# Kernel tuning notes

Hardware: AMD Instinct MI355X
Metric: run time of the kernel (lower is better)

Reference implementation:

```python
import jax, jax.numpy as jnp
import numpy as np

T_LATENCY = 2  # refractory latency (timesteps), from init_kwargs
FS_SCALE = 10.0  # FastSigmoid surrogate scale


@jax.custom_vjp
def fast_sigmoid_spike(u):
    return (u > 0).astype(u.dtype)

def _fs_fwd(u):
    return fast_sigmoid_spike(u), u

def _fs_bwd(u, g):
    return (g / (FS_SCALE * jnp.abs(u) + 1.0) ** 2,)

fast_sigmoid_spike.defvjp(_fs_fwd, _fs_bwd)


def setup_inputs() -> dict:
    key = jax.random.key(0)
    k1, k2, k3, k4 = jax.random.split(key, 4)
    B, N, T = 64, 1024, 512
    x = jax.random.normal(k1, (B, N, T), dtype=jnp.float32)
    beta = jax.random.uniform(k2, (N,), jnp.float32, 0.3, 0.95)   # leak
    p = jax.random.uniform(k3, (N,), jnp.float32, 0.5, 0.95)      # adaptation decay
    b = jax.random.uniform(k4, (N,), jnp.float32, 0.5, 1.5)       # adaptation strength
    return {"x": x, "beta": beta, "p": p, "b": b}


def reference(x, beta, p, b):
    # clamped effective params (matches torch @property accessors)
    beta_c = jnp.clip(beta, 0.001, 0.999)
    p_c = jnp.clip(jnp.abs(p), 0.0, 0.999)
    b_c = jnp.clip(jnp.abs(b), 0.001, 1.0)

    B, N, T = x.shape
    xt = jnp.moveaxis(x, 2, 0)  # [T, B, N]

    def step(carry, x_t):
        mem, spikes, refac, a, v_th = carry
        # spike-triggered refractory reset, then mask input during refractory window
        refac = jnp.where(spikes > 0, 0.0, refac)
        ic = jnp.where(refac < T_LATENCY, 0.0, x_t)
        refac = refac + 1.0
        # leaky integration
        new_mem = mem * beta_c + ic
        s = fast_sigmoid_spike(new_mem - v_th)
        # reset-by-subtraction-to-zero with detached spikes (detach_spike_grad=True)
        mem = new_mem * (1.0 - jax.lax.stop_gradient(s))
        # adaptive threshold
        a = p_c * a + s
        v_th = 1.0 + b_c * a
        return (mem, s, refac, a, v_th), s

    z = jnp.zeros((B, N), x.dtype)
    init = (z, z, jnp.full((B, N), float(T_LATENCY), x.dtype), z,
            jnp.ones((B, N), x.dtype))
    _, spikes_seq = jax.lax.scan(step, init, xt)  # [T, B, N]
    return jnp.moveaxis(spikes_seq, 0, 2)  # [B, N, T]
```

## Files before the change

kernel.cpp:

```cpp
#include <hip/hip_runtime.h>

#pragma clang fp contract(off)

#define ROWS    64
#define T_LEN   512
#define CHUNK   64
#define NCHUNK  (T_LEN / CHUNK)
#define STRIDE  (CHUNK + 4)
#define NVEC    (ROWS * CHUNK / 4 / ROWS)
#define NPARAM  1024

__global__ __launch_bounds__(ROWS) void snn_fwd(
    const float* __restrict__ x,
    const float* __restrict__ beta,
    const float* __restrict__ p,
    const float* __restrict__ bparam,
    float* __restrict__ out)
{
    __shared__ float inbuf[ROWS * STRIDE];
    __shared__ float outbuf[ROWS * STRIDE];

    const int tid     = threadIdx.x;
    const int rowBase = blockIdx.x * ROWS;
    const int n       = (rowBase + tid) & (NPARAM - 1);

    const float beta_c = fminf(fmaxf(beta[n], 0.001f), 0.999f);
    const float p_c    = fminf(fabsf(p[n]), 0.999f);
    const float b_c    = fminf(fmaxf(fabsf(bparam[n]), 0.001f), 1.0f);

    float mem = 0.0f, refac = 2.0f, a = 0.0f, vth = 1.0f, ps = 0.0f;

    const float4* __restrict__ xv = (const float4*)x;
    float4* __restrict__ ov       = (float4*)out;

    const int t4c   = tid & 15;
    const int rquad = tid >> 4;
    const int gq    = (rowBase + rquad) * (T_LEN / 4) + t4c;
    const int lq    = rquad * STRIDE + t4c * 4;

    float4 ld[NVEC];

    auto loadChunk = [&](int k) {
        const int base = gq + k * (CHUNK / 4);
        #pragma unroll
        for (int it = 0; it < NVEC; ++it)
            ld[it] = xv[base + it * 4 * (T_LEN / 4)];
    };

    auto stage = [&]() {
        #pragma unroll
        for (int it = 0; it < NVEC; ++it)
            *(float4*)&inbuf[lq + it * 4 * STRIDE] = ld[it];
    };

    auto readout = [&](int k) {
        const int base = gq + k * (CHUNK / 4);
        #pragma unroll
        for (int it = 0; it < NVEC; ++it) {
            float4 sv = *(const float4*)&outbuf[lq + it * 4 * STRIDE];
            ov[base + it * 4 * (T_LEN / 4)] = sv;
        }
    };

    auto step = [&](float xt) -> float {
        refac = (ps > 0.0f) ? 0.0f : refac;
        const float ic = (refac < 2.0f) ? 0.0f : xt;
        refac += 1.0f;
        const float nm   = __fadd_rn(__fmul_rn(mem, beta_c), ic);
        const float diff = __fsub_rn(nm, vth);
        const float s    = (diff > 0.0f) ? 1.0f : 0.0f;
        mem = (diff > 0.0f) ? 0.0f : nm;
        a   = __fadd_rn(__fmul_rn(p_c, a), s);
        vth = __fadd_rn(1.0f, __fmul_rn(b_c, a));
        ps  = s;
        return s;
    };

    loadChunk(0);
    const int cbase = tid * STRIDE;

    #pragma unroll 1
    for (int k = 0; k < NCHUNK; ++k) {
        stage();
        if (k > 0) readout(k - 1);
        __syncthreads();
        if (k + 1 < NCHUNK) loadChunk(k + 1);
        #pragma unroll
        for (int t4 = 0; t4 < CHUNK / 4; ++t4) {
            float4 xq = *(const float4*)&inbuf[cbase + t4 * 4];
            float4 sv;
            sv.x = step(xq.x);
            sv.y = step(xq.y);
            sv.z = step(xq.z);
            sv.w = step(xq.w);
            *(float4*)&outbuf[cbase + t4 * 4] = sv;
        }
        __syncthreads();
    }
    readout(NCHUNK - 1);
}

extern "C" void kernel_launch(void* const* d_in, const int* in_sizes, int n_in,
                              void* d_out, int out_size, void* d_ws, size_t ws_size,
                              hipStream_t stream) {
    const float* x    = (const float*)d_in[0];
    const float* beta = (const float*)d_in[1];
    const float* p    = (const float*)d_in[2];
    const float* b    = (const float*)d_in[3];
    float* out        = (float*)d_out;

    const int BN = 64 * 1024;
    snn_fwd<<<dim3(BN / ROWS), dim3(ROWS), 0, stream>>>(x, beta, p, b, out);
}
```

Baseline: 260.9 us.

## Warp-specialize block into compute, loader and store wavefronts with double buffering

The block grows from one to three wavefronts. Wave 0 runs the serial recurrence, wave 1 prefetches and stages the next input chunk into a double-buffered shared array, and wave 2 drains the previous output chunk to global memory. The chunk size is halved to 32 timesteps. The goal is to take global load and store latency off the compute wave's critical path, at the cost of extra threads, twice the shared memory and more block barriers per row group.

```diff
diff --git a/kernel.cpp b/kernel.cpp
--- a/kernel.cpp
+++ b/kernel.cpp
@@ -4,63 +4,45 @@
 
 #define ROWS    64
 #define T_LEN   512
-#define CHUNK   64
+#define CHUNK   32
 #define NCHUNK  (T_LEN / CHUNK)
 #define STRIDE  (CHUNK + 4)
-#define NVEC    (ROWS * CHUNK / 4 / ROWS)
+#define NV      8
 #define NPARAM  1024
 
-__global__ __launch_bounds__(ROWS) void snn_fwd(
+__global__ __launch_bounds__(192) void snn_fwd(
     const float* __restrict__ x,
     const float* __restrict__ beta,
     const float* __restrict__ p,
     const float* __restrict__ bparam,
     float* __restrict__ out)
 {
-    __shared__ float inbuf[ROWS * STRIDE];
-    __shared__ float outbuf[ROWS * STRIDE];
+    __shared__ __align__(16) float inbuf [2][ROWS * STRIDE];
+    __shared__ __align__(16) float outbuf[2][ROWS * STRIDE];
 
     const int tid     = threadIdx.x;
+    const int wid     = tid >> 6;
+    const int lane    = tid & 63;
     const int rowBase = blockIdx.x * ROWS;
-    const int n       = (rowBase + tid) & (NPARAM - 1);
-
-    const float beta_c = fminf(fmaxf(beta[n], 0.001f), 0.999f);
-    const float p_c    = fminf(fabsf(p[n]), 0.999f);
-    const float b_c    = fminf(fmaxf(fabsf(bparam[n]), 0.001f), 1.0f);
-
-    float mem = 0.0f, refac = 2.0f, a = 0.0f, vth = 1.0f, ps = 0.0f;
 
     const float4* __restrict__ xv = (const float4*)x;
     float4* __restrict__ ov       = (float4*)out;
 
-    const int t4c   = tid & 15;
-    const int rquad = tid >> 4;
-    const int gq    = (rowBase + rquad) * (T_LEN / 4) + t4c;
-    const int lq    = rquad * STRIDE + t4c * 4;
+    const int t8 = lane & 7;
+    const int r8 = lane >> 3;
+    const int gq = (rowBase + r8) * (T_LEN / 4) + t8;
+    const int lq = r8 * STRIDE + t8 * 4;
 
-    float4 ld[NVEC];
+    float mem = 0.0f, refac = 2.0f, a = 0.0f, vth = 1.0f, ps = 0.0f;
+    float beta_c = 0.f, p_c = 0.f, b_c = 0.f;
+    const int cbase = lane * STRIDE;
 
-    auto loadChunk = [&](int k) {
-        const int base = gq + k * (CHUNK / 4);
-        #pragma unroll
-        for (int it = 0; it < NVEC; ++it)
-            ld[it] = xv[base + it * 4 * (T_LEN / 4)];
-    };
-
-    auto stage = [&]() {
-        #pragma unroll
-        for (int it = 0; it < NVEC; ++it)
-            *(float4*)&inbuf[lq + it * 4 * STRIDE] = ld[it];
-    };
-
-    auto readout = [&](int k) {
-        const int base = gq + k * (CHUNK / 4);
-        #pragma unroll
-        for (int it = 0; it < NVEC; ++it) {
-            float4 sv = *(const float4*)&outbuf[lq + it * 4 * STRIDE];
-            ov[base + it * 4 * (T_LEN / 4)] = sv;
-        }
-    };
+    if (wid == 0) {
+        const int n = (rowBase + lane) & (NPARAM - 1);
+        beta_c = fminf(fmaxf(beta[n], 0.001f), 0.999f);
+        p_c    = fminf(fabsf(p[n]), 0.999f);
+        b_c    = fminf(fmaxf(fabsf(bparam[n]), 0.001f), 1.0f);
+    }
 
     auto step = [&](float xt) -> float {
         refac = (ps > 0.0f) ? 0.0f : refac;
@@ -76,28 +58,60 @@
         return s;
     };
 
-    loadChunk(0);
-    const int cbase = tid * STRIDE;
+    float4 ld[NV];
+
+    auto loadChunk = [&](int k) {
+        const int base = gq + k * (CHUNK / 4);
+        #pragma unroll
+        for (int it = 0; it < NV; ++it)
+            ld[it] = xv[base + it * 8 * (T_LEN / 4)];
+    };
+    auto stage = [&](int buf) {
+        #pragma unroll
+        for (int it = 0; it < NV; ++it)
+            *(float4*)&inbuf[buf][lq + it * 8 * STRIDE] = ld[it];
+    };
+    auto drain = [&](int buf, int k) {
+        float4 sv[NV];
+        #pragma unroll
+        for (int it = 0; it < NV; ++it)
+            sv[it] = *(const float4*)&outbuf[buf][lq + it * 8 * STRIDE];
+        const int base = gq + k * (CHUNK / 4);
+        #pragma unroll
+        for (int it = 0; it < NV; ++it)
+            ov[base + it * 8 * (T_LEN / 4)] = sv[it];
+    };
+
+    if (wid == 1) {
+        loadChunk(0);
+        stage(0);
+        loadChunk(1);
+    }
+    __syncthreads();
 
     #pragma unroll 1
     for (int k = 0; k < NCHUNK; ++k) {
-        stage();
-        if (k > 0) readout(k - 1);
-        __syncthreads();
-        if (k + 1 < NCHUNK) loadChunk(k + 1);
-        #pragma unroll
-        for (int t4 = 0; t4 < CHUNK / 4; ++t4) {
-            float4 xq = *(const float4*)&inbuf[cbase + t4 * 4];
-            float4 sv;
-            sv.x = step(xq.x);
-            sv.y = step(xq.y);
-            sv.z = step(xq.z);
-            sv.w = step(xq.w);
-            *(float4*)&outbuf[cbase + t4 * 4] = sv;
+        const int cur = k & 1;
+        if (wid == 0) {
+            #pragma unroll
+            for (int t4 = 0; t4 < CHUNK / 4; ++t4) {
+                float4 xq = *(const float4*)&inbuf[cur][cbase + t4 * 4];
+                float4 sv;
+                sv.x = step(xq.x);
+                sv.y = step(xq.y);
+                sv.z = step(xq.z);
+                sv.w = step(xq.w);
+                *(float4*)&outbuf[cur][cbase + t4 * 4] = sv;
+            }
+        } else if (wid == 1) {
+            if (k + 1 < NCHUNK) stage(cur ^ 1);
+            if (k + 2 < NCHUNK) loadChunk(k + 2);
+        } else {
+            if (k > 0) drain(cur ^ 1, k - 1);
         }
         __syncthreads();
     }
-    readout(NCHUNK - 1);
+    if (wid == 2) drain(1, NCHUNK - 1);
 }
 
 extern "C" void kernel_launch(void* const* d_in, const int* in_sizes, int n_in,
@@ -110,5 +124,5 @@
     float* out        = (float*)d_out;
 
     const int BN = 64 * 1024;
-    snn_fwd<<<dim3(BN / ROWS), dim3(ROWS), 0, stream>>>(x, beta, p, b, out);
+    snn_fwd<<<dim3(BN / ROWS), dim3(192), 0, stream>>>(x, beta, p, b, out);
 }
```

Measured after the change: 253.6 us. 1.03x faster.
